# Kernel tuning notes

Hardware: AMD Instinct MI355X
Metric: run time of the kernel (lower is better)

The kernel has to match this reference:

```python
import jax, jax.numpy as jnp
import numpy as np

CHUNK = 4        # rows per split
IN_F = 72        # 4*6*3 flattened chunk
OUT_F = 1800     # linear output, viewed as (180,5,2)


def setup_inputs() -> dict:
    key = jax.random.key(0)
    k1, k2, k3 = jax.random.split(key, 3)
    N = 262144  # multiple of 4, so torch's zero-padding of the last chunk is a no-op
    x = jax.random.normal(k1, (N, 6, 3), dtype=jnp.float32)
    W = jax.random.normal(k2, (OUT_F, IN_F), dtype=jnp.float32) * (1.0 / np.sqrt(IN_F))
    b = jax.random.normal(k3, (OUT_F,), dtype=jnp.float32) * 0.01
    return {"x": x, "W": W, "b": b}


def reference(x, W, b):
    # Original: for each split of 4 rows of [6,3], pad to (4,6,3), flatten to 72,
    # Linear(72,1800) + ReLU, view (180,5,2); concatenate all chunks.
    # Vectorized: reshape to [n_chunks, 72] and do one batched GEMM.
    n = x.shape[0]
    n_chunks = -(-n // CHUNK)
    pad = n_chunks * CHUNK - n
    if pad:
        x = jnp.concatenate([x, jnp.zeros((pad, 6, 3), dtype=x.dtype)], axis=0)
    flat = x.reshape(n_chunks, IN_F)                       # [C, 72]
    h = jax.nn.relu(jnp.einsum('ci,oi->co', flat, W) + b)  # [C, 1800]
    # torch returns torch.split(cat, 180): equivalent to the concatenated array
    return h.reshape(n_chunks * 180, 5, 2)
```

## Files before the change

kernel.cpp:

```cpp
#include <hip/hip_runtime.h>
#include <hip/hip_bf16.h>


typedef __bf16 bf16;
typedef bf16  bf16x4 __attribute__((ext_vector_type(4)));
typedef bf16  bf16x8 __attribute__((ext_vector_type(8)));
typedef float f32x4  __attribute__((ext_vector_type(4)));

#define KDIM   72
#define NDIM   1800
#define MTILES 1024
#define NSEG   64

__global__ __launch_bounds__(256, 4)
void edges_mlp_kernel(const float* __restrict__ A,
                      const float* __restrict__ W,
                      const float* __restrict__ bias,
                      float* __restrict__ out)
{
    __shared__ bf16 Bs[64][104];

    const int t  = threadIdx.x;
    const int n0 = blockIdx.x * 64;

    for (int idx = t; idx < 64 * 3; idx += 256) {
        int r = idx / 3, p = idx % 3;
        *(uint4*)((char*)&Bs[r][0] + KDIM * 2 + p * 16) = make_uint4(0u, 0u, 0u, 0u);
    }
    for (int i = t; i < 64 * 18; i += 256) {
        int n = i / 18, q = i % 18;
        int gn = n0 + n;
        float4 v = make_float4(0.f, 0.f, 0.f, 0.f);
        if (gn < NDIM) v = *(const float4*)(W + (size_t)gn * KDIM + q * 4);
        bf16x4 h = { (bf16)v.x, (bf16)v.y, (bf16)v.z, (bf16)v.w };
        *(bf16x4*)&Bs[n][q * 4] = h;
    }
    __syncthreads();

    const int wave = t >> 6;
    const int lane = t & 63;
    const int lrow = lane & 15;
    const int hi   = lane >> 4;

    bf16x8 bfrag[3][4];
    #pragma unroll
    for (int ks = 0; ks < 3; ++ks)
        #pragma unroll
        for (int nt = 0; nt < 4; ++nt)
            bfrag[ks][nt] = *(const bf16x8*)&Bs[nt * 16 + lrow][ks * 32 + hi * 8];

    float bv[4];
    #pragma unroll
    for (int nt = 0; nt < 4; ++nt) {
        int col = n0 + nt * 16 + lrow;
        bv[nt] = (col < NDIM) ? bias[col] : 0.f;
    }

    const int arow_in_tile = wave * 16 + lrow;

    for (int mt = blockIdx.y; mt < MTILES; mt += NSEG) {
        const size_t m0 = (size_t)mt * 64;
        const float* arow = A + (m0 + arow_in_tile) * KDIM;

        bf16x8 afrag[3];
        #pragma unroll
        for (int ks = 0; ks < 3; ++ks) {
            const int k0 = ks * 32 + hi * 8;
            float av[8];
            if (k0 < KDIM) {
                float4 u0 = *(const float4*)(arow + k0);
                float4 u1 = *(const float4*)(arow + k0 + 4);
                av[0] = u0.x; av[1] = u0.y; av[2] = u0.z; av[3] = u0.w;
                av[4] = u1.x; av[5] = u1.y; av[6] = u1.z; av[7] = u1.w;
            } else {
                #pragma unroll
                for (int j = 0; j < 8; ++j) av[j] = 0.f;
            }
            bf16x8 h;
            #pragma unroll
            for (int j = 0; j < 8; ++j) h[j] = (bf16)av[j];
            afrag[ks] = h;
        }

        f32x4 acc[4] = { {0,0,0,0}, {0,0,0,0}, {0,0,0,0}, {0,0,0,0} };
        #pragma unroll
        for (int ks = 0; ks < 3; ++ks)
            #pragma unroll
            for (int nt = 0; nt < 4; ++nt)
                acc[nt] = __builtin_amdgcn_mfma_f32_16x16x32_bf16(afrag[ks], bfrag[ks][nt], acc[nt], 0, 0, 0);

        const size_t orow0 = m0 + wave * 16 + hi * 4;
        #pragma unroll
        for (int nt = 0; nt < 4; ++nt) {
            int col = n0 + nt * 16 + lrow;
            if (col < NDIM) {
                #pragma unroll
                for (int r = 0; r < 4; ++r) {
                    float v = fmaxf(acc[nt][r] + bv[nt], 0.0f);
                    __builtin_nontemporal_store(v, &out[(orow0 + r) * NDIM + col]);
                }
            }
        }
    }
}

extern "C" void kernel_launch(void* const* d_in, const int* in_sizes, int n_in,
                              void* d_out, int out_size, void* d_ws, size_t ws_size,
                              hipStream_t stream) {
    const float* x = (const float*)d_in[0];
    const float* W = (const float*)d_in[1];
    const float* b = (const float*)d_in[2];
    float* out = (float*)d_out;

    dim3 grid((NDIM + 63) / 64, NSEG);
    edges_mlp_kernel<<<grid, 256, 0, stream>>>(x, W, b, out);
}
```

Baseline: 708.0 us.

## Pre-swizzle W to MFMA fragment layout and transpose output tiles for float4 stores

Adds a prep kernel that converts W to bf16 in MFMA fragment order in workspace, plus a padded bias copy. The main kernel now gives each block 64 rows of A and loops over all N chunks, reading W fragments straight from global memory (L2-resident) instead of staging them through shared memory. Swapping the MFMA operands puts each lane's accumulator along contiguous output columns, so results go out as float4 stores instead of scalar nontemporal stores. It adds two extra launches and repeated global W reads per block, and the stores are no longer nontemporal.

```diff
diff --git a/kernel.cpp b/kernel.cpp
--- a/kernel.cpp
+++ b/kernel.cpp
@@ -3,102 +3,99 @@
 
 
 typedef __bf16 bf16;
-typedef bf16  bf16x4 __attribute__((ext_vector_type(4)));
 typedef bf16  bf16x8 __attribute__((ext_vector_type(8)));
 typedef float f32x4  __attribute__((ext_vector_type(4)));
 
-#define KDIM   72
-#define NDIM   1800
-#define MTILES 1024
-#define NSEG   64
+#define KDIM    72
+#define NDIM    1800
+#define NCHUNK  29
+#define NFRAG   (NCHUNK * 4)
+#define WB_BYTES (NFRAG * 3 * 64 * 8 * 2)
+#define BIAS_OFF WB_BYTES
+#define NPAD    1856
+
+__global__ void swizzle_W_kernel(const float* __restrict__ W, bf16* __restrict__ Wb) {
+    int idx = blockIdx.x * 256 + threadIdx.x;
+    if (idx >= NFRAG * 3 * 64) return;
+    int lane = idx & 63;
+    int ks   = (idx >> 6) % 3;
+    int frag = idx / 192;
+    int n  = frag * 16 + (lane & 15);
+    int k0 = ks * 32 + (lane >> 4) * 8;
+    bf16x8 h = {0,0,0,0,0,0,0,0};
+    if (n < NDIM && k0 < KDIM) {
+        const float* p = W + (size_t)n * KDIM + k0;
+        float4 u0 = *(const float4*)p;
+        float4 u1 = *(const float4*)(p + 4);
+        h[0]=(bf16)u0.x; h[1]=(bf16)u0.y; h[2]=(bf16)u0.z; h[3]=(bf16)u0.w;
+        h[4]=(bf16)u1.x; h[5]=(bf16)u1.y; h[6]=(bf16)u1.z; h[7]=(bf16)u1.w;
+    }
+    *((bf16x8*)Wb + idx) = h;
+}
+
+__global__ void pad_bias_kernel(const float* __restrict__ b, float* __restrict__ bp) {
+    int i = blockIdx.x * 256 + threadIdx.x;
+    if (i < NPAD) bp[i] = (i < NDIM) ? b[i] : 0.f;
+}
 
 __global__ __launch_bounds__(256, 4)
 void edges_mlp_kernel(const float* __restrict__ A,
-                      const float* __restrict__ W,
-                      const float* __restrict__ bias,
+                      const bf16*  __restrict__ Wb,
+                      const float* __restrict__ biasp,
                       float* __restrict__ out)
 {
-    __shared__ bf16 Bs[64][104];
-
-    const int t  = threadIdx.x;
-    const int n0 = blockIdx.x * 64;
-
-    for (int idx = t; idx < 64 * 3; idx += 256) {
-        int r = idx / 3, p = idx % 3;
-        *(uint4*)((char*)&Bs[r][0] + KDIM * 2 + p * 16) = make_uint4(0u, 0u, 0u, 0u);
-    }
-    for (int i = t; i < 64 * 18; i += 256) {
-        int n = i / 18, q = i % 18;
-        int gn = n0 + n;
-        float4 v = make_float4(0.f, 0.f, 0.f, 0.f);
-        if (gn < NDIM) v = *(const float4*)(W + (size_t)gn * KDIM + q * 4);
-        bf16x4 h = { (bf16)v.x, (bf16)v.y, (bf16)v.z, (bf16)v.w };
-        *(bf16x4*)&Bs[n][q * 4] = h;
-    }
-    __syncthreads();
-
+    const int t    = threadIdx.x;
     const int wave = t >> 6;
     const int lane = t & 63;
-    const int lrow = lane & 15;
     const int hi   = lane >> 4;
 
-    bf16x8 bfrag[3][4];
+    const size_t m = (size_t)blockIdx.x * 64 + wave * 16 + (lane & 15);
+
+    const float* arow = A + m * KDIM;
+    bf16x8 afrag[3];
     #pragma unroll
-    for (int ks = 0; ks < 3; ++ks)
+    for (int ks = 0; ks < 3; ++ks) {
+        const int k0 = ks * 32 + hi * 8;
+        bf16x8 h = {0,0,0,0,0,0,0,0};
+        if (k0 < KDIM) {
+            float4 u0 = *(const float4*)(arow + k0);
+            float4 u1 = *(const float4*)(arow + k0 + 4);
+            h[0]=(bf16)u0.x; h[1]=(bf16)u0.y; h[2]=(bf16)u0.z; h[3]=(bf16)u0.w;
+            h[4]=(bf16)u1.x; h[5]=(bf16)u1.y; h[6]=(bf16)u1.z; h[7]=(bf16)u1.w;
+        }
+        afrag[ks] = h;
+    }
+
+    const bf16x8* wp = (const bf16x8*)Wb + lane;
+    float* orow = out + m * NDIM;
+
+    for (int nc = 0; nc < NCHUNK; ++nc) {
+        bf16x8 wfr[3][4];
         #pragma unroll
         for (int nt = 0; nt < 4; ++nt)
-            bfrag[ks][nt] = *(const bf16x8*)&Bs[nt * 16 + lrow][ks * 32 + hi * 8];
-
-    float bv[4];
-    #pragma unroll
-    for (int nt = 0; nt < 4; ++nt) {
-        int col = n0 + nt * 16 + lrow;
-        bv[nt] = (col < NDIM) ? bias[col] : 0.f;
-    }
-
-    const int arow_in_tile = wave * 16 + lrow;
-
-    for (int mt = blockIdx.y; mt < MTILES; mt += NSEG) {
-        const size_t m0 = (size_t)mt * 64;
-        const float* arow = A + (m0 + arow_in_tile) * KDIM;
-
-        bf16x8 afrag[3];
-        #pragma unroll
-        for (int ks = 0; ks < 3; ++ks) {
-            const int k0 = ks * 32 + hi * 8;
-            float av[8];
-            if (k0 < KDIM) {
-                float4 u0 = *(const float4*)(arow + k0);
-                float4 u1 = *(const float4*)(arow + k0 + 4);
-                av[0] = u0.x; av[1] = u0.y; av[2] = u0.z; av[3] = u0.w;
-                av[4] = u1.x; av[5] = u1.y; av[6] = u1.z; av[7] = u1.w;
-            } else {
-                #pragma unroll
-                for (int j = 0; j < 8; ++j) av[j] = 0.f;
-            }
-            bf16x8 h;
             #pragma unroll
-            for (int j = 0; j < 8; ++j) h[j] = (bf16)av[j];
-            afrag[ks] = h;
-        }
+            for (int ks = 0; ks < 3; ++ks)
+                wfr[ks][nt] = wp[((size_t)(nc * 4 + nt) * 3 + ks) * 64];
 
         f32x4 acc[4] = { {0,0,0,0}, {0,0,0,0}, {0,0,0,0}, {0,0,0,0} };
         #pragma unroll
         for (int ks = 0; ks < 3; ++ks)
             #pragma unroll
             for (int nt = 0; nt < 4; ++nt)
-                acc[nt] = __builtin_amdgcn_mfma_f32_16x16x32_bf16(afrag[ks], bfrag[ks][nt], acc[nt], 0, 0, 0);
+                acc[nt] = __builtin_amdgcn_mfma_f32_16x16x32_bf16(wfr[ks][nt], afrag[ks], acc[nt], 0, 0, 0);
 
-        const size_t orow0 = m0 + wave * 16 + hi * 4;
+        const int nb = nc * 64 + hi * 4;
         #pragma unroll
         for (int nt = 0; nt < 4; ++nt) {
-            int col = n0 + nt * 16 + lrow;
-            if (col < NDIM) {
-                #pragma unroll
-                for (int r = 0; r < 4; ++r) {
-                    float v = fmaxf(acc[nt][r] + bv[nt], 0.0f);
-                    __builtin_nontemporal_store(v, &out[(orow0 + r) * NDIM + col]);
-                }
+            int n = nb + nt * 16;
+            if (n + 3 < NDIM) {
+                float4 bb = *(const float4*)(biasp + n);
+                float4 v;
+                v.x = fmaxf(acc[nt][0] + bb.x, 0.f);
+                v.y = fmaxf(acc[nt][1] + bb.y, 0.f);
+                v.z = fmaxf(acc[nt][2] + bb.z, 0.f);
+                v.w = fmaxf(acc[nt][3] + bb.w, 0.f);
+                *(float4*)(orow + n) = v;
             }
         }
     }
@@ -112,6 +109,12 @@
     const float* b = (const float*)d_in[2];
     float* out = (float*)d_out;
 
-    dim3 grid((NDIM + 63) / 64, NSEG);
-    edges_mlp_kernel<<<grid, 256, 0, stream>>>(x, W, b, out);
+    bf16*  Wb    = (bf16*)d_ws;
+    float* biasp = (float*)((char*)d_ws + BIAS_OFF);
+
+    swizzle_W_kernel<<<(NFRAG * 3 * 64 + 255) / 256, 256, 0, stream>>>(W, Wb);
+    pad_bias_kernel<<<(NPAD + 255) / 256, 256, 0, stream>>>(b, biasp);
+
+    const int chunks = in_sizes[0] / KDIM;
+    edges_mlp_kernel<<<chunks / 64, 256, 0, stream>>>(x, Wb, biasp, out);
 }
```

Result: faster. 619.5 us (-12.5%).
